# Performance work log

Measured on AMD Instinct MI355X. Metric: run time of the kernel, lower is better.

The kernel has to match this reference:

```python
import jax, jax.numpy as jnp
import numpy as np

EPS = 1e-5

def setup_inputs() -> dict:
    key = jax.random.key(0)
    ks = jax.random.split(key, 12)
    b, C, Hx = 8, 1024, 28          # x: (b, C, Hx, Hx); y: (b, C//2, 2*Hx, 2*Hx)
    C2 = C // 2
    r = C2 // 7                      # fc bottleneck = 73
    f32 = jnp.float32
    inp = {
        'y': jax.random.normal(ks[0], (b, C2, 2*Hx, 2*Hx), f32),
        'x': jax.random.normal(ks[1], (b, C, Hx, Hx), f32),
        'fc1_w': jax.random.normal(ks[2], (r, C2), f32) * 0.02,
        'fc2_w': jax.random.normal(ks[3], (C2, r), f32) * 0.02,
        'conv_w': jax.random.normal(ks[4], (C2, C, 1, 1), f32) * 0.02,
        'conv_b': jnp.zeros((C2,), f32),
        'conv1_w': jax.random.normal(ks[5], (C2, C2 * 4, 1, 1), f32) * 0.02,
        'conv1_b': jnp.zeros((C2,), f32),
        'bn_gamma': jnp.ones((C2,), f32),
        'bn_beta': jnp.zeros((C2,), f32),
        'bn_mean': jnp.zeros((C2,), f32),
        'bn_var': jnp.ones((C2,), f32),
        'dw_w': jax.random.normal(ks[6], (C, 1, 3, 3), f32) * 0.1,  # depthwise, groups=C
        'dw_b': jnp.zeros((C,), f32),
    }
    return inp

def reference(y, x, fc1_w, fc2_w, conv_w, conv_b, conv1_w, conv1_b,
              bn_gamma, bn_beta, bn_mean, bn_var, dw_w, dw_b):
    def bn(t):  # BatchNorm2d in eval mode (running stats); same bn module reused twice
        return (t - bn_mean[:, None, None]) * jax.lax.rsqrt(bn_var[:, None, None] + EPS) \
               * bn_gamma[:, None, None] + bn_beta[:, None, None]
    # SE channel attention on y
    s = jnp.mean(y, axis=(2, 3))                              # (b, C2) GAP
    s = jax.nn.relu(s @ fc1_w.T) @ fc2_w.T                    # bias-free FCs
    y1 = y * jax.nn.sigmoid(s)[:, :, None, None]
    # depthwise 3x3 conv on x
    x1 = jax.lax.conv_general_dilated(
        x, dw_w, (1, 1), ((1, 1), (1, 1)),
        feature_group_count=x.shape[1],
        dimension_numbers=('NCHW', 'OIHW', 'NCHW')) + dw_b[None, :, None, None]
    # np.cov per (b, c) map: rows are variables, ddof=1 -> (Xc @ Xc^T)/(W-1)
    Wn = x1.shape[-1]
    xc = x1 - jnp.mean(x1, axis=-1, keepdims=True)
    x2 = jnp.einsum('bchw,bcgw->bchg', xc, xc) / (Wn - 1)     # (b, C, H, H)
    # 1x1 conv C->C2, bn, sigmoid
    x2 = jnp.einsum('bchw,oc->bohw', x2, conv_w[:, :, 0, 0]) + conv_b[None, :, None, None]
    x2 = jax.nn.sigmoid(bn(x2))
    # bilinear upsample x2 (half-pixel == torch align_corners=False)
    def up2(t):
        bb, cc, hh, ww = t.shape
        return jax.image.resize(t, (bb, cc, 2 * hh, 2 * ww), method='bilinear')
    x_up = up2(x)
    x2_up = up2(x2)
    cat = jnp.concatenate([y1, x2_up, x_up], axis=1)          # (b, 4*C2, 2H, 2W)
    out = jnp.einsum('bchw,oc->bohw', cat, conv1_w[:, :, 0, 0]) + conv1_b[None, :, None, None]
    return jax.nn.relu(bn(out))
```

## Files before the change

kernel.cpp:

```cpp
#include <hip/hip_runtime.h>
#include <math.h>

#define EPSV 1e-5f
#define B 8
#define C 1024
#define C2 512
#define RK 73
#define HW 784
#define QW 3136

typedef __attribute__((ext_vector_type(8))) short bf16x8;
typedef __attribute__((ext_vector_type(4))) float f32x4;

__device__ __forceinline__ unsigned short f2bf(float f) {
    unsigned u = __float_as_uint(f);
    return (unsigned short)((u + 0x7fffu + ((u >> 16) & 1u)) >> 16);
}
__device__ __forceinline__ unsigned cvt_pk_bf16(float lo, float hi) {
    unsigned r;
    asm("v_cvt_pk_bf16_f32 %0, %1, %2" : "=v"(r) : "v"(lo), "v"(hi));
    return r;
}
__device__ __forceinline__ float ld_f(const float* p) { return *p; }
__device__ __forceinline__ float ld_f(const unsigned short* p) {
    return __uint_as_float(((unsigned)*p) << 16);
}

__global__ void gap_kernel(const float* __restrict__ y, float* __restrict__ s0) {
    int bc = blockIdx.x;
    const float* p = y + (size_t)bc * QW;
    float sum = 0.f;
    for (int i = threadIdx.x; i < QW; i += 256) sum += p[i];
    for (int off = 32; off > 0; off >>= 1) sum += __shfl_down(sum, off, 64);
    __shared__ float red[4];
    if ((threadIdx.x & 63) == 0) red[threadIdx.x >> 6] = sum;
    __syncthreads();
    if (threadIdx.x == 0)
        s0[bc] = (red[0] + red[1] + red[2] + red[3]) * (1.0f / QW);
}

__global__ void se_fc_kernel(const float* __restrict__ s0,
                             const float* __restrict__ fc1_w,
                             const float* __restrict__ fc2_w,
                             float* __restrict__ att) {
    int b = blockIdx.x;
    __shared__ float sv[C2];
    __shared__ float hv[RK];
    for (int i = threadIdx.x; i < C2; i += 256) sv[i] = s0[b * C2 + i];
    __syncthreads();
    if (threadIdx.x < RK) {
        float acc = 0.f;
        const float* wr = fc1_w + threadIdx.x * C2;
        for (int k = 0; k < C2; ++k) acc += wr[k] * sv[k];
        hv[threadIdx.x] = fmaxf(acc, 0.f);
    }
    __syncthreads();
    for (int o = threadIdx.x; o < C2; o += 256) {
        float acc = 0.f;
        const float* wr = fc2_w + o * RK;
        for (int j = 0; j < RK; ++j) acc += wr[j] * hv[j];
        att[b * C2 + o] = 1.f / (1.f + expf(-acc));
    }
}

__global__ void dwcov_kernel(const float* __restrict__ x,
                             const float* __restrict__ dw_w,
                             const float* __restrict__ dw_b,
                             unsigned short* __restrict__ cov) {
    int bc = blockIdx.x;
    int c = bc & (C - 1);
    __shared__ float xs[HW];
    __shared__ float x1[HW];
    __shared__ float rm[28];
    const float* px = x + (size_t)bc * HW;
    for (int i = threadIdx.x; i < HW; i += 256) xs[i] = px[i];
    float wk[9];
#pragma unroll
    for (int j = 0; j < 9; ++j) wk[j] = dw_w[c * 9 + j];
    float bias = dw_b[c];
    __syncthreads();
    for (int p = threadIdx.x; p < HW; p += 256) {
        int h = p / 28, w = p - h * 28;
        float acc = bias;
#pragma unroll
        for (int dh = 0; dh < 3; ++dh) {
            int hh = h + dh - 1;
            if (hh < 0 || hh >= 28) continue;
#pragma unroll
            for (int dw = 0; dw < 3; ++dw) {
                int ww = w + dw - 1;
                if (ww < 0 || ww >= 28) continue;
                acc += xs[hh * 28 + ww] * wk[dh * 3 + dw];
            }
        }
        x1[p] = acc;
    }
    __syncthreads();
    if (threadIdx.x < 28) {
        float s = 0.f;
        for (int w = 0; w < 28; ++w) s += x1[threadIdx.x * 28 + w];
        rm[threadIdx.x] = s * (1.f / 28.f);
    }
    __syncthreads();
    unsigned short* pc = cov + (size_t)bc * HW;
    for (int p = threadIdx.x; p < HW; p += 256) {
        int h = p / 28, g = p - h * 28;
        float mh = rm[h], mg = rm[g];
        float acc = 0.f;
        for (int w = 0; w < 28; ++w)
            acc += (x1[h * 28 + w] - mh) * (x1[g * 28 + w] - mg);
        pc[p] = f2bf(acc * (1.f / 27.f));
    }
}

__global__ void pack_w(const float* __restrict__ conv_w, const float* __restrict__ conv_b,
                       const float* __restrict__ conv1_w, const float* __restrict__ conv1_b,
                       const float* __restrict__ bn_g, const float* __restrict__ bn_b,
                       const float* __restrict__ bn_m, const float* __restrict__ bn_v,
                       const float* __restrict__ att,
                       unsigned short* __restrict__ w0b, unsigned short* __restrict__ w1y,
                       unsigned short* __restrict__ w1pT,
                       float* __restrict__ sA, float* __restrict__ sB0, float* __restrict__ sB1) {
    int o = blockIdx.x, t = threadIdx.x;
    for (int i = t; i < C; i += 256) w0b[(size_t)o * C + i] = f2bf(conv_w[(size_t)o * C + i]);
    for (int i = t; i < 1536; i += 256) w1pT[(size_t)o * 1536 + i] = f2bf(conv1_w[(size_t)o * 2048 + 512 + i]);
#pragma unroll
    for (int b = 0; b < B; ++b)
        for (int c = t; c < C2; c += 256)
            w1y[((size_t)b * C2 + o) * C2 + c] = f2bf(conv1_w[(size_t)o * 2048 + c] * att[b * C2 + c]);
    if (t == 0) {
        float sc = rsqrtf(bn_v[o] + EPSV) * bn_g[o];
        float bi = bn_b[o] - bn_m[o] * sc;
        sA[o] = sc;
        sB0[o] = conv_b[o] * sc + bi;
        sB1[o] = conv1_b[o] * sc + bi;
    }
}

__global__ __launch_bounds__(256)
void transpose_pass(const float* __restrict__ src, unsigned short* __restrict__ dst,
                    int rows, int cols, int dpitch, int doff) {
    int b = blockIdx.z;
    int c0 = blockIdx.y * 64, p0 = blockIdx.x * 64;
    __shared__ float ts[64][65];
    int tid = threadIdx.x;
    int pl = tid & 63, r0 = tid >> 6;
    const float* sb = src + ((size_t)b * rows + c0) * cols + p0;
    if (p0 + pl < cols) {
#pragma unroll
        for (int j = 0; j < 16; ++j) {
            int cl = r0 + j * 4;
            ts[cl][pl] = sb[(size_t)cl * cols + pl];
        }
    }
    __syncthreads();
    int cl = tid & 63;
#pragma unroll
    for (int j = 0; j < 16; ++j) {
        int pl2 = r0 + j * 4;
        if (p0 + pl2 < cols)
            dst[((size_t)b * cols + p0 + pl2) * dpitch + doff + c0 + cl] = f2bf(ts[cl][pl2]);
    }
}

template<int MODE, int K>
__global__ __launch_bounds__(256)
void mfma_gemm(const unsigned short* __restrict__ wpk,
               const void* __restrict__ bsrc_v,
               const unsigned short* __restrict__ Pb,
               const float* __restrict__ sA, const float* __restrict__ sB,
               void* __restrict__ outv) {
    constexpr int NIT = K / 32;
    constexpr int NT  = (MODE == 2) ? 49 : 98;
    constexpr int QN = NT >> 3, REM = NT & 7;
    int bx = blockIdx.x;
    int r = bx & 7, ii = bx >> 3;
    int og = ii & 7, s = ii >> 3;
    int cnt = QN + (r < REM ? 1 : 0);
    if (s >= cnt) return;
    int t = (r < REM ? r * (QN + 1) : REM * (QN + 1) + (r - REM) * QN) + s;
    int o0 = og * 64;
    int n0 = t * 64;
    int b = blockIdx.z;
    union SM {
        struct { __align__(16) unsigned short Wt[2][2560]; __align__(16) unsigned short At[2][2560]; } s;
        float pt[(MODE == 2) ? 64 * 84 : 4];
    };
    __shared__ SM sm;
    int tid = threadIdx.x;
    int lane = tid & 63, wv = tid >> 6;
    int ln = lane & 15, quad = lane >> 4;
    int o_w = (wv >> 1) * 32, q_w = (wv & 1) * 32;
    int swr = tid >> 2, swk = (tid & 3) * 8;
    int s_gq = tid & 63, s_gk8 = tid >> 6;
    int qg = n0 + s_gq;
    const unsigned short* wp = (MODE == 2) ? wpk + (size_t)b * C2 * C2 : wpk;
    const unsigned short* wg = wp + (size_t)(o0 + swr) * K + swk;
    const unsigned short* bg_s = nullptr;
    const unsigned short* bg_c = nullptr;
    const float* bg_f = nullptr;
    if (MODE == 0) {
        int bq = qg / HW, pp = qg - bq * HW;
        bg_s = (const unsigned short*)bsrc_v + ((size_t)bq * C + s_gk8 * 8) * HW + pp;
    } else if (MODE == 1) {
        bg_c = (const unsigned short*)bsrc_v + (size_t)(n0 + swr) * K + swk;
    } else {
        bg_f = (const float*)bsrc_v + ((size_t)b * C2 + s_gk8 * 8) * QW + qg;
    }

    uint4 stA_a, stB_a;
    uint4 stA_b, stB_b;
    unsigned stA_h[8], stB_h[8];
    float stA_f[8], stB_f[8];

#define LD_STAGE(P, CH) {                                                   \
        P##_a = *(const uint4*)(wg + (size_t)(CH) * 32);                    \
        if (MODE == 0) {                                                    \
            const unsigned short* _p = bg_s + (size_t)(CH) * 32 * HW;       \
            _Pragma("unroll")                                               \
            for (int _j = 0; _j < 8; ++_j) P##_h[_j] = _p[(size_t)_j * HW]; \
        } else if (MODE == 1) {                                             \
            P##_b = *(const uint4*)(bg_c + (size_t)(CH) * 32);              \
        } else {                                                            \
            const float* _p = bg_f + (size_t)(CH) * 32 * QW;                \
            _Pragma("unroll")                                               \
            for (int _j = 0; _j < 8; ++_j) P##_f[_j] = _p[(size_t)_j * QW]; \
        } }

#define ST_STAGE(P, BUF) {                                                  \
        *(uint4*)&sm.s.Wt[BUF][swr * 40 + swk] = P##_a;                     \
        if (MODE == 1) {                                                    \
            *(uint4*)&sm.s.At[BUF][swr * 40 + swk] = P##_b;                 \
        } else if (MODE == 0) {                                             \
            uint4 _v;                                                       \
            _v.x = P##_h[0] | (P##_h[1] << 16);                             \
            _v.y = P##_h[2] | (P##_h[3] << 16);                             \
            _v.z = P##_h[4] | (P##_h[5] << 16);                             \
            _v.w = P##_h[6] | (P##_h[7] << 16);                             \
            *(uint4*)&sm.s.At[BUF][s_gq * 40 + s_gk8 * 8] = _v;             \
        } else {                                                            \
            uint4 _v;                                                       \
            _v.x = cvt_pk_bf16(P##_f[0], P##_f[1]);                         \
            _v.y = cvt_pk_bf16(P##_f[2], P##_f[3]);                         \
            _v.z = cvt_pk_bf16(P##_f[4], P##_f[5]);                         \
            _v.w = cvt_pk_bf16(P##_f[6], P##_f[7]);                         \
            *(uint4*)&sm.s.At[BUF][s_gq * 40 + s_gk8 * 8] = _v;             \
        } }

#define GEMM_BODY(BUF, P, CHW, CHL) {                                               \
        bf16x8 af0 = *(const bf16x8*)&sm.s.Wt[BUF][(o_w + ln) * 40 + quad * 8];     \
        bf16x8 af1 = *(const bf16x8*)&sm.s.Wt[BUF][(o_w + 16 + ln) * 40 + quad * 8];\
        bf16x8 bf0 = *(const bf16x8*)&sm.s.At[BUF][(q_w + ln) * 40 + quad * 8];     \
        bf16x8 bf1 = *(const bf16x8*)&sm.s.At[BUF][(q_w + 16 + ln) * 40 + quad * 8];\
        acc[0][0] = __builtin_amdgcn_mfma_f32_16x16x32_bf16(af0, bf0, acc[0][0], 0, 0, 0); \
        acc[0][1] = __builtin_amdgcn_mfma_f32_16x16x32_bf16(af0, bf1, acc[0][1], 0, 0, 0); \
        acc[1][0] = __builtin_amdgcn_mfma_f32_16x16x32_bf16(af1, bf0, acc[1][0], 0, 0, 0); \
        acc[1][1] = __builtin_amdgcn_mfma_f32_16x16x32_bf16(af1, bf1, acc[1][1], 0, 0, 0); \
        if ((CHW) < NIT) {                                                          \
            ST_STAGE(P, (BUF) ^ 1)                                                  \
            if ((CHL) < NIT) LD_STAGE(P, (CHL))                                     \
            asm volatile("s_waitcnt lgkmcnt(0)" ::: "memory");                      \
            __builtin_amdgcn_s_barrier();                                           \
            __builtin_amdgcn_sched_barrier(0);                                      \
        } }

    LD_STAGE(stA, 0)
    ST_STAGE(stA, 0)
    LD_STAGE(stA, 1)
    if (2 < NIT) LD_STAGE(stB, 2)
    asm volatile("s_waitcnt lgkmcnt(0)" ::: "memory");
    __builtin_amdgcn_s_barrier();
    __builtin_amdgcn_sched_barrier(0);

    f32x4 acc[2][2] = {};
    for (int i2 = 0; i2 < NIT; i2 += 2) {
        GEMM_BODY(0, stA, i2 + 1, i2 + 3)
        GEMM_BODY(1, stB, i2 + 2, i2 + 4)
    }
#undef GEMM_BODY
#undef ST_STAGE
#undef LD_STAGE

    if (MODE == 2) {
        float* outp = (float*)outv;
        __syncthreads();
        int h0 = n0 / 56;
        int hmin = (h0 & 1) ? (h0 >> 1) : max(0, (h0 >> 1) - 1);
        for (int e = tid; e < 64 * 84; e += 256) {
            int o_l = e / 84, rem = e - o_l * 84;
            int s2 = rem / 28, w = rem - s2 * 28;
            int row = min(hmin + s2, 27);
            sm.pt[e] = ld_f(&Pb[((size_t)b * C2 + o0 + o_l) * HW + row * 28 + w]);
        }
        __syncthreads();
#pragma unroll
        for (int nt = 0; nt < 2; ++nt) {
            int q = n0 + q_w + nt * 16 + ln;
            int hq = q / 56, wq = q - hq * 56;
            int hm = hq >> 1, wm = wq >> 1;
            int hn = (hq & 1) ? min(hm + 1, 27) : max(hm - 1, 0);
            int wn_ = (wq & 1) ? min(wm + 1, 27) : max(wm - 1, 0);
            int rm_ = (hm - hmin) * 28, rn_ = (hn - hmin) * 28;
#pragma unroll
            for (int mt = 0; mt < 2; ++mt)
#pragma unroll
                for (int reg = 0; reg < 4; ++reg) {
                    int ol = o_w + mt * 16 + quad * 4 + reg;
                    int o = o0 + ol;
                    const float* Pt = &sm.pt[ol * 84];
                    float up = 0.5625f * Pt[rm_ + wm] + 0.1875f * (Pt[rm_ + wn_] + Pt[rn_ + wm])
                             + 0.0625f * Pt[rn_ + wn_];
                    float v = (acc[mt][nt][reg] + up) * sA[o] + sB[o];
                    outp[((size_t)b * C2 + o) * QW + q] = fmaxf(v, 0.f);
                }
        }
    } else if (MODE == 0) {
        unsigned short* outp = (unsigned short*)outv;
#pragma unroll
        for (int nt = 0; nt < 2; ++nt) {
            int n = n0 + q_w + nt * 16 + ln;
#pragma unroll
            for (int mt = 0; mt < 2; ++mt) {
                int ob = o0 + o_w + mt * 16 + quad * 4;
                unsigned short pk[4];
#pragma unroll
                for (int reg = 0; reg < 4; ++reg) {
                    int o = ob + reg;
                    float v = acc[mt][nt][reg] * sA[o] + sB[o];
                    pk[reg] = f2bf(1.f / (1.f + expf(-v)));
                }
                *(uint2*)&outp[(size_t)n * 1536 + ob] = *(uint2*)pk;
            }
        }
    } else {
        unsigned short* outp = (unsigned short*)outv;
#pragma unroll
        for (int nt = 0; nt < 2; ++nt) {
            int n = n0 + q_w + nt * 16 + ln;
            int be = n / HW, pe = n - be * HW;
#pragma unroll
            for (int mt = 0; mt < 2; ++mt)
#pragma unroll
                for (int reg = 0; reg < 4; ++reg) {
                    int o = o0 + o_w + mt * 16 + quad * 4 + reg;
                    outp[((size_t)be * C2 + o) * HW + pe] = f2bf(acc[mt][nt][reg]);
                }
        }
    }
}

extern "C" void kernel_launch(void* const* d_in, const int* in_sizes, int n_in,
                              void* d_out, int out_size, void* d_ws, size_t ws_size,
                              hipStream_t stream) {
    const float* y       = (const float*)d_in[0];
    const float* x       = (const float*)d_in[1];
    const float* fc1_w   = (const float*)d_in[2];
    const float* fc2_w   = (const float*)d_in[3];
    const float* conv_w  = (const float*)d_in[4];
    const float* conv_b  = (const float*)d_in[5];
    const float* conv1_w = (const float*)d_in[6];
    const float* conv1_b = (const float*)d_in[7];
    const float* bn_g    = (const float*)d_in[8];
    const float* bn_b    = (const float*)d_in[9];
    const float* bn_m    = (const float*)d_in[10];
    const float* bn_v    = (const float*)d_in[11];
    const float* dw_w    = (const float*)d_in[12];
    const float* dw_b    = (const float*)d_in[13];
    float* out = (float*)d_out;

    float* ws  = (float*)d_ws;
    float* s0  = ws;
    float* att = ws + 4096;
    float* sA  = ws + 8192;
    float* sB0 = ws + 8704;
    float* sB1 = ws + 9216;
    unsigned short* w0b    = (unsigned short*)(ws + 9728);
    unsigned short* w1y    = w0b + (size_t)C2 * C;
    unsigned short* w1pT   = w1y + (size_t)B * C2 * C2;
    unsigned short* cov_bf = w1pT + (size_t)C2 * 1536;
    unsigned short* BcatT  = cov_bf + (size_t)B * C * HW;
    unsigned short* Pb     = BcatT + (size_t)B * HW * 1536;

    gap_kernel<<<B * C2, 256, 0, stream>>>(y, s0);
    se_fc_kernel<<<B, 256, 0, stream>>>(s0, fc1_w, fc2_w, att);
    pack_w<<<C2, 256, 0, stream>>>(conv_w, conv_b, conv1_w, conv1_b,
                                   bn_g, bn_b, bn_m, bn_v, att,
                                   w0b, w1y, w1pT, sA, sB0, sB1);
    dwcov_kernel<<<B * C, 256, 0, stream>>>(x, dw_w, dw_b, cov_bf);
    transpose_pass<<<dim3(13, 16, B), 256, 0, stream>>>(x, BcatT, C, HW, 1536, 512);
    mfma_gemm<0, 1024><<<dim3(832), 256, 0, stream>>>(w0b, cov_bf, nullptr, sA, sB0, BcatT);
    mfma_gemm<1, 1536><<<dim3(832), 256, 0, stream>>>(w1pT, BcatT, nullptr, sA, sB0, Pb);
    mfma_gemm<2, 512><<<dim3(448, 1, B), 256, 0, stream>>>(w1y, y, Pb, sA, sB1, out);
}
```

Before: 320.3 us.

## Pre-transpose GEMM B operands so all MFMA modes use vectorized loads

Adds separate transpose passes for the covariance maps and for y (with the SE attention folded in during the transpose). The GEMMs can then load the B operand with contiguous 16-byte loads instead of strided per-element gathers. Attention now scales activations, not per-batch weights. Scratch buffers are placed in the output buffer. This costs extra kernels and extra full read/write passes over cov and y, in exchange for cheaper, coalesced loads inside the GEMMs.

```diff
diff --git a/kernel.cpp b/kernel.cpp
--- a/kernel.cpp
+++ b/kernel.cpp
@@ -15,11 +15,6 @@
 __device__ __forceinline__ unsigned short f2bf(float f) {
     unsigned u = __float_as_uint(f);
     return (unsigned short)((u + 0x7fffu + ((u >> 16) & 1u)) >> 16);
-}
-__device__ __forceinline__ unsigned cvt_pk_bf16(float lo, float hi) {
-    unsigned r;
-    asm("v_cvt_pk_bf16_f32 %0, %1, %2" : "=v"(r) : "v"(lo), "v"(hi));
-    return r;
 }
 __device__ __forceinline__ float ld_f(const float* p) { return *p; }
 __device__ __forceinline__ float ld_f(const unsigned short* p) {
@@ -117,17 +112,13 @@
                        const float* __restrict__ conv1_w, const float* __restrict__ conv1_b,
                        const float* __restrict__ bn_g, const float* __restrict__ bn_b,
                        const float* __restrict__ bn_m, const float* __restrict__ bn_v,
-                       const float* __restrict__ att,
-                       unsigned short* __restrict__ w0b, unsigned short* __restrict__ w1y,
+                       unsigned short* __restrict__ w0b, unsigned short* __restrict__ w1p0,
                        unsigned short* __restrict__ w1pT,
                        float* __restrict__ sA, float* __restrict__ sB0, float* __restrict__ sB1) {
     int o = blockIdx.x, t = threadIdx.x;
     for (int i = t; i < C; i += 256) w0b[(size_t)o * C + i] = f2bf(conv_w[(size_t)o * C + i]);
+    for (int i = t; i < C2; i += 256) w1p0[(size_t)o * C2 + i] = f2bf(conv1_w[(size_t)o * 2048 + i]);
     for (int i = t; i < 1536; i += 256) w1pT[(size_t)o * 1536 + i] = f2bf(conv1_w[(size_t)o * 2048 + 512 + i]);
-#pragma unroll
-    for (int b = 0; b < B; ++b)
-        for (int c = t; c < C2; c += 256)
-            w1y[((size_t)b * C2 + o) * C2 + c] = f2bf(conv1_w[(size_t)o * 2048 + c] * att[b * C2 + c]);
     if (t == 0) {
         float sc = rsqrtf(bn_v[o] + EPSV) * bn_g[o];
         float bi = bn_b[o] - bn_m[o] * sc;
@@ -137,36 +128,39 @@
     }
 }
 
+template<typename ST, bool ATT>
 __global__ __launch_bounds__(256)
-void transpose_pass(const float* __restrict__ src, unsigned short* __restrict__ dst,
+void transpose_pass(const ST* __restrict__ src, unsigned short* __restrict__ dst,
+                    const float* __restrict__ att,
                     int rows, int cols, int dpitch, int doff) {
     int b = blockIdx.z;
     int c0 = blockIdx.y * 64, p0 = blockIdx.x * 64;
     __shared__ float ts[64][65];
     int tid = threadIdx.x;
     int pl = tid & 63, r0 = tid >> 6;
-    const float* sb = src + ((size_t)b * rows + c0) * cols + p0;
+    const ST* sb = src + ((size_t)b * rows + c0) * cols + p0;
     if (p0 + pl < cols) {
 #pragma unroll
         for (int j = 0; j < 16; ++j) {
             int cl = r0 + j * 4;
-            ts[cl][pl] = sb[(size_t)cl * cols + pl];
+            ts[cl][pl] = ld_f(&sb[(size_t)cl * cols + pl]);
         }
     }
     __syncthreads();
     int cl = tid & 63;
+    float av = ATT ? att[b * rows + c0 + cl] : 1.f;
 #pragma unroll
     for (int j = 0; j < 16; ++j) {
         int pl2 = r0 + j * 4;
         if (p0 + pl2 < cols)
-            dst[((size_t)b * cols + p0 + pl2) * dpitch + doff + c0 + cl] = f2bf(ts[cl][pl2]);
+            dst[((size_t)b * cols + p0 + pl2) * dpitch + doff + c0 + cl] = f2bf(ts[cl][pl2] * av);
     }
 }
 
 template<int MODE, int K>
 __global__ __launch_bounds__(256)
 void mfma_gemm(const unsigned short* __restrict__ wpk,
-               const void* __restrict__ bsrc_v,
+               const unsigned short* __restrict__ bsrc,
                const unsigned short* __restrict__ Pb,
                const float* __restrict__ sA, const float* __restrict__ sB,
                void* __restrict__ outv) {
@@ -192,60 +186,18 @@
     int ln = lane & 15, quad = lane >> 4;
     int o_w = (wv >> 1) * 32, q_w = (wv & 1) * 32;
     int swr = tid >> 2, swk = (tid & 3) * 8;
-    int s_gq = tid & 63, s_gk8 = tid >> 6;
-    int qg = n0 + s_gq;
-    const unsigned short* wp = (MODE == 2) ? wpk + (size_t)b * C2 * C2 : wpk;
-    const unsigned short* wg = wp + (size_t)(o0 + swr) * K + swk;
-    const unsigned short* bg_s = nullptr;
-    const unsigned short* bg_c = nullptr;
-    const float* bg_f = nullptr;
-    if (MODE == 0) {
-        int bq = qg / HW, pp = qg - bq * HW;
-        bg_s = (const unsigned short*)bsrc_v + ((size_t)bq * C + s_gk8 * 8) * HW + pp;
-    } else if (MODE == 1) {
-        bg_c = (const unsigned short*)bsrc_v + (size_t)(n0 + swr) * K + swk;
-    } else {
-        bg_f = (const float*)bsrc_v + ((size_t)b * C2 + s_gk8 * 8) * QW + qg;
-    }
-
-    uint4 stA_a, stB_a;
-    uint4 stA_b, stB_b;
-    unsigned stA_h[8], stB_h[8];
-    float stA_f[8], stB_f[8];
+    const unsigned short* wg = wpk + (size_t)(o0 + swr) * K + swk;
+    const unsigned short* bg = bsrc + ((size_t)((MODE == 2) ? b * QW : 0) + n0 + swr) * K + swk;
+
+    uint4 stA_a, stA_b, stB_a, stB_b;
 
 #define LD_STAGE(P, CH) {                                                   \
         P##_a = *(const uint4*)(wg + (size_t)(CH) * 32);                    \
-        if (MODE == 0) {                                                    \
-            const unsigned short* _p = bg_s + (size_t)(CH) * 32 * HW;       \
-            _Pragma("unroll")                                               \
-            for (int _j = 0; _j < 8; ++_j) P##_h[_j] = _p[(size_t)_j * HW]; \
-        } else if (MODE == 1) {                                             \
-            P##_b = *(const uint4*)(bg_c + (size_t)(CH) * 32);              \
-        } else {                                                            \
-            const float* _p = bg_f + (size_t)(CH) * 32 * QW;                \
-            _Pragma("unroll")                                               \
-            for (int _j = 0; _j < 8; ++_j) P##_f[_j] = _p[(size_t)_j * QW]; \
-        } }
+        P##_b = *(const uint4*)(bg + (size_t)(CH) * 32); }
 
 #define ST_STAGE(P, BUF) {                                                  \
         *(uint4*)&sm.s.Wt[BUF][swr * 40 + swk] = P##_a;                     \
-        if (MODE == 1) {                                                    \
-            *(uint4*)&sm.s.At[BUF][swr * 40 + swk] = P##_b;                 \
-        } else if (MODE == 0) {                                             \
-            uint4 _v;                                                       \
-            _v.x = P##_h[0] | (P##_h[1] << 16);                             \
-            _v.y = P##_h[2] | (P##_h[3] << 16);                             \
-            _v.z = P##_h[4] | (P##_h[5] << 16);                             \
-            _v.w = P##_h[6] | (P##_h[7] << 16);                             \
-            *(uint4*)&sm.s.At[BUF][s_gq * 40 + s_gk8 * 8] = _v;             \
-        } else {                                                            \
-            uint4 _v;                                                       \
-            _v.x = cvt_pk_bf16(P##_f[0], P##_f[1]);                         \
-            _v.y = cvt_pk_bf16(P##_f[2], P##_f[3]);                         \
-            _v.z = cvt_pk_bf16(P##_f[4], P##_f[5]);                         \
-            _v.w = cvt_pk_bf16(P##_f[6], P##_f[7]);                         \
-            *(uint4*)&sm.s.At[BUF][s_gq * 40 + s_gk8 * 8] = _v;             \
-        } }
+        *(uint4*)&sm.s.At[BUF][swr * 40 + swk] = P##_b; }
 
 #define GEMM_BODY(BUF, P, CHW, CHL) {                                               \
         bf16x8 af0 = *(const bf16x8*)&sm.s.Wt[BUF][(o_w + ln) * 40 + quad * 8];     \
@@ -267,7 +219,7 @@
     LD_STAGE(stA, 0)
     ST_STAGE(stA, 0)
     LD_STAGE(stA, 1)
-    if (2 < NIT) LD_STAGE(stB, 2)
+    LD_STAGE(stB, 2)
     asm volatile("s_waitcnt lgkmcnt(0)" ::: "memory");
     __builtin_amdgcn_s_barrier();
     __builtin_amdgcn_sched_barrier(0);
@@ -368,27 +320,35 @@
     const float* dw_b    = (const float*)d_in[13];
     float* out = (float*)d_out;
 
+    unsigned short* cov_bf = (unsigned short*)d_out;
+    unsigned short* covT   = cov_bf + (size_t)B * C * HW;
+    unsigned short* BcatT  = covT + (size_t)B * HW * C;
+
     float* ws  = (float*)d_ws;
     float* s0  = ws;
     float* att = ws + 4096;
     float* sA  = ws + 8192;
     float* sB0 = ws + 8704;
     float* sB1 = ws + 9216;
-    unsigned short* w0b    = (unsigned short*)(ws + 9728);
-    unsigned short* w1y    = w0b + (size_t)C2 * C;
-    unsigned short* w1pT   = w1y + (size_t)B * C2 * C2;
-    unsigned short* cov_bf = w1pT + (size_t)C2 * 1536;
-    unsigned short* BcatT  = cov_bf + (size_t)B * C * HW;
-    unsigned short* Pb     = BcatT + (size_t)B * HW * 1536;
+    unsigned short* w0b  = (unsigned short*)(ws + 9728);
+    unsigned short* w1p0 = w0b + (size_t)C2 * C;
+    unsigned short* w1pT = w1p0 + (size_t)C2 * C2;
+    unsigned short* yT   = w1pT + (size_t)C2 * 1536;
+    unsigned short* Pb   = yT + (size_t)B * QW * C2;
 
     gap_kernel<<<B * C2, 256, 0, stream>>>(y, s0);
     se_fc_kernel<<<B, 256, 0, stream>>>(s0, fc1_w, fc2_w, att);
     pack_w<<<C2, 256, 0, stream>>>(conv_w, conv_b, conv1_w, conv1_b,
-                                   bn_g, bn_b, bn_m, bn_v, att,
-                                   w0b, w1y, w1pT, sA, sB0, sB1);
+                                   bn_g, bn_b, bn_m, bn_v,
+                                   w0b, w1p0, w1pT, sA, sB0, sB1);
     dwcov_kernel<<<B * C, 256, 0, stream>>>(x, dw_w, dw_b, cov_bf);
-    transpose_pass<<<dim3(13, 16, B), 256, 0, stream>>>(x, BcatT, C, HW, 1536, 512);
-    mfma_gemm<0, 1024><<<dim3(832), 256, 0, stream>>>(w0b, cov_bf, nullptr, sA, sB0, BcatT);
+    transpose_pass<float, false><<<dim3(13, 16, B), 256, 0, stream>>>(
+        x, BcatT, nullptr, C, HW, 1536, 512);
+    transpose_pass<unsigned short, false><<<dim3(13, 16, B), 256, 0, stream>>>(
+        cov_bf, covT, nullptr, C, HW, C, 0);
+    transpose_pass<float, true><<<dim3(49, 8, B), 256, 0, stream>>>(
+        y, yT, att, C2, QW, C2, 0);
+    mfma_gemm<0, 1024><<<dim3(832), 256, 0, stream>>>(w0b, covT, nullptr, sA, sB0, BcatT);
     mfma_gemm<1, 1536><<<dim3(832), 256, 0, stream>>>(w1pT, BcatT, nullptr, sA, sB0, Pb);
-    mfma_gemm<2, 512><<<dim3(448, 1, B), 256, 0, stream>>>(w1y, y, Pb, sA, sB1, out);
-}
+    mfma_gemm<2, 512><<<dim3(448, 1, B), 256, 0, stream>>>(w1p0, yT, Pb, sA, sB1, out);
+}
```

Measured after the change: 328.0 us. 2.4% more time.
